# Kernel optimization log

Measured on AMD Instinct MI355X. Metric: run time of the kernel, lower is better.

The kernel has to match this reference:

```python
import jax, jax.numpy as jnp
import numpy as np

KS = 7001          # Gaussian kernel taps (hard-coded in smooth_predictions)
STD = 30.0
B, S, D = 512, 8000, 256


def gaussian_kernel():
    # torch.linspace(-size//2 + 1, size//2, size) with size=7001 -> -3500..3500
    x = jnp.linspace(-(KS // 2), KS // 2, KS)
    k = jnp.exp(-x ** 2 / (2.0 * STD ** 2))
    return k / jnp.sum(k)


def smooth_predictions(v):
    # v: (B, 1, S); depthwise (single-channel) conv1d, 'same' padding
    k = gaussian_kernel().reshape(1, 1, KS).astype(v.dtype)
    return jax.lax.conv_general_dilated(
        v, k, window_strides=(1,), padding=[(KS // 2, KS // 2)],
        dimension_numbers=('NCH', 'OIH', 'NCH'))


def _param(b, w, bias, lo, hi):
    # Linear(D,1) -> relu -> clamp; returns (B, 1)
    return jnp.clip(jax.nn.relu(b @ w.T + bias), lo, hi)


def setup_inputs() -> dict:
    key = jax.random.key(0)
    ks = jax.random.split(key, 10)
    inp = {
        'v_out': jax.random.normal(ks[0], (B, 1, S), jnp.float32),
        'b': jax.random.normal(ks[1], (B, D), jnp.float32),
        'k_w': 0.02 * jax.random.normal(ks[2], (1, D), jnp.float32),
        'k_b': jnp.zeros((1,), jnp.float32),
        'a_w': 0.02 * jax.random.normal(ks[3], (1, D), jnp.float32),
        'a_b': jnp.zeros((1,), jnp.float32),
        'epsilon_w': 0.02 * jax.random.normal(ks[4], (1, D), jnp.float32),
        'epsilon_b': jnp.zeros((1,), jnp.float32),
        'gamma_w': 0.02 * jax.random.normal(ks[5], (1, D), jnp.float32),
        'gamma_b': jnp.zeros((1,), jnp.float32),
        'use_cond': 0,
        'name': 0,
    }
    return inp


def reference(v_out, b, k_w, k_b, a_w, a_b, epsilon_w, epsilon_b,
              gamma_w, gamma_b, use_cond, name):
    t_ = jnp.ones_like(v_out) * 1.6            # (B,1,S)
    t_out = t_                                  # expanded form is identical

    k = _param(b, k_w, k_b, 0.1, 1.0)          # (B,1)
    a = _param(b, a_w, a_b, 0.001, 0.1)
    epsilon = _param(b, epsilon_w, epsilon_b, 0.005, 0.1)
    gamma = _param(b, gamma_w, gamma_b, 0.5, 2.0)

    # unsqueeze(1) + expand over seq -> broadcast as (B,1,1)
    k_e = k[:, :, None]
    a_e = a[:, :, None]
    eps_e = epsilon[:, :, None]
    g_e = gamma[:, :, None]

    ones = jnp.ones_like(v_out)
    v_s = smooth_predictions(v_out)            # (B,1,S)

    dv_l = jnp.pad(v_s, ((0, 0), (0, 0), (1, 0)))   # (B,1,S+1)
    dv_r = jnp.pad(v_s, ((0, 0), (0, 0), (0, 1)))   # (B,1,S+1)
    dt = t_out / 7999.0
    dv_t = (dv_r[:, :, 1:] - dv_l[:, :, :-1]) / (2.0 * dt)
    dv2_t = (dv_r[:, :, 1:] + dv_l[:, :, :-1] - 2.0 * v_s) / dt ** 2

    eps_0 = 0.001
    v_noisy = jnp.where(v_s == 0, jnp.full_like(v_s, eps_0), v_s)
    inv_v = v_noisy ** (-1)
    inv_v = jnp.where(jnp.isnan(inv_v), jnp.zeros_like(inv_v), inv_v)

    term_l1 = v_s * k_e * dv_t * (ones - 2.0 * v_s + a_e)
    term_l2 = inv_v * dv_t ** 2
    term_lt = 1000.0 * term_l1 + term_l2 - dv2_t

    term_r1 = v_s * (v_s - g_e * k_e * 1000.0 * (ones - v_s) * (v_s - a_e))
    term_rt = eps_e * (term_r1 + g_e * dv_t)

    dv_out = term_lt - term_rt
    if use_cond:
        dv_out = jnp.where(v_out <= 0, jnp.zeros_like(dv_out), dv_out)

    dv_out = jnp.concatenate([dv_out[:, :, 100:950], dv_out[:, :, 1050:-100]],
                             axis=2)
    dv_out = jnp.log(dv_out ** 2 + 1e-5)
    return (dv_out, dv_t, dv2_t, a, k * 1000.0, epsilon, gamma, t_,
            dv_l, dv_r, t_out)
```

## Files before the change

kernel.cpp:

```cpp
#include <hip/hip_runtime.h>
#include <math.h>

#define SLEN 8000
#define NBATCH 512
#define DDIM 256

#define RAD 160
#define TAPS (2 * RAD + 1)
#define CHUNK 2048
#define CBLK 256
#define TPO 8
#define WIN (CHUNK + 2 * RAD + 16)
#define LDSZ (WIN + WIN / 8)

#define O0  0
#define O1  3942400
#define O2  8038400
#define O3  12134400
#define O4  12134912
#define O5  12135424
#define O6  12135936
#define O7  12136448
#define O8  16232448
#define O9  20328960
#define O10 24425472

struct WTable { float w[TAPS]; };

__global__ __launch_bounds__(256) void pc_params_kernel(
    const float* __restrict__ b,
    const float* __restrict__ kw, const float* __restrict__ kb,
    const float* __restrict__ aw, const float* __restrict__ ab,
    const float* __restrict__ ew, const float* __restrict__ eb,
    const float* __restrict__ gw, const float* __restrict__ gb,
    float* __restrict__ out3, float* __restrict__ out4,
    float* __restrict__ out5, float* __restrict__ out6,
    float* __restrict__ wsp)
{
    __shared__ float4 red[256];
    const int row = blockIdx.x;
    const int d = threadIdx.x;
    const float bv = b[row * DDIM + d];
    red[d] = make_float4(bv * kw[d], bv * aw[d], bv * ew[d], bv * gw[d]);
    __syncthreads();
    for (int s2 = 128; s2 > 0; s2 >>= 1) {
        if (d < s2) {
            float4 o = red[d + s2];
            red[d].x += o.x; red[d].y += o.y; red[d].z += o.z; red[d].w += o.w;
        }
        __syncthreads();
    }
    if (d == 0) {
        float4 s = red[0];
        float k = fminf(fmaxf(fmaxf(s.x + kb[0], 0.0f), 0.1f),   1.0f);
        float a = fminf(fmaxf(fmaxf(s.y + ab[0], 0.0f), 0.001f), 0.1f);
        float e = fminf(fmaxf(fmaxf(s.z + eb[0], 0.0f), 0.005f), 0.1f);
        float g = fminf(fmaxf(fmaxf(s.w + gb[0], 0.0f), 0.5f),   2.0f);
        out3[row] = a;
        out4[row] = k * 1000.0f;
        out5[row] = e;
        out6[row] = g;
        wsp[row]          = k;
        wsp[512 + row]    = a;
        wsp[1024 + row]   = e;
        wsp[1536 + row]   = g;
    }
}

__global__ __launch_bounds__(CBLK) void pc_conv_kernel(
    const float* __restrict__ v,
    float* __restrict__ dvl,
    float* __restrict__ dvr,
    WTable wt)
{
    __shared__ float lds[LDSZ];
    const int row = blockIdx.y;
    const int i0 = blockIdx.x * CHUNK;
    const int tid = threadIdx.x;
    const float* vrow = v + row * SLEN;

    for (int idx = tid; idx < WIN; idx += CBLK) {
        const int g = i0 - RAD + idx;
        const float val = (g >= 0 && g < SLEN) ? vrow[g] : 0.0f;
        lds[idx + (idx >> 3)] = val;
    }
    __syncthreads();

    const int base = tid * TPO;
    float acc[TPO];
#pragma unroll
    for (int t = 0; t < TPO; ++t) acc[t] = 0.0f;

    float sreg[16];
    const float* p0 = lds + 9 * tid;
#pragma unroll
    for (int k = 0; k < 8; ++k) sreg[k] = p0[k];
#pragma unroll
    for (int k = 0; k < 8; ++k) sreg[8 + k] = p0[9 + k];

#pragma unroll 2
    for (int jb = 0; jb < TAPS - 1; jb += 8) {
#pragma unroll
        for (int c = 0; c < 8; ++c) {
            const float wc = wt.w[jb + c];
#pragma unroll
            for (int t = 0; t < TPO; ++t) acc[t] += wc * sreg[c + t];
        }
#pragma unroll
        for (int k = 0; k < 8; ++k) sreg[k] = sreg[k + 8];
        const float* pn = lds + 9 * tid + 9 * ((jb >> 3) + 2);
#pragma unroll
        for (int k = 0; k < 8; ++k) sreg[8 + k] = pn[k];
    }
    {
        const float wc = wt.w[TAPS - 1];
#pragma unroll
        for (int t = 0; t < TPO; ++t) acc[t] += wc * sreg[t];
    }

    const long rb = (long)row * 8001;
#pragma unroll
    for (int t = 0; t < TPO; ++t) {
        const int i = i0 + base + t;
        if (i < SLEN) {
            dvr[rb + i] = acc[t];
            dvl[rb + i + 1] = acc[t];
            if (i == 0) dvl[rb] = 0.0f;
            if (i == SLEN - 1) dvr[rb + SLEN] = 0.0f;
        }
    }
}

__global__ __launch_bounds__(256) void pc_pointwise_kernel(
    const float* __restrict__ dvr,
    const float* __restrict__ wsp,
    const float* __restrict__ v_out,
    const int* __restrict__ use_cond,
    float* __restrict__ out0, float* __restrict__ out1,
    float* __restrict__ out2, float* __restrict__ out7,
    float* __restrict__ out10)
{
    const int row = blockIdx.y;
    const int i = blockIdx.x * 256 + threadIdx.x;
    if (i >= SLEN) return;
    const long rb = (long)row * 8001;

    const float vc = dvr[rb + i];
    const float vm = (i > 0) ? dvr[rb + i - 1] : 0.0f;
    const float vp = dvr[rb + i + 1];

    const float kk = wsp[row];
    const float aa = wsp[512 + row];
    const float ee = wsp[1024 + row];
    const float gg = wsp[1536 + row];

    constexpr float DT = 1.6f / 7999.0f;
    constexpr float C1 = 1.0f / (2.0f * DT);
    constexpr float C2 = 1.0f / (DT * DT);

    const float dv_t = (vp - vm) * C1;
    const float dv2  = (vp + vm - 2.0f * vc) * C2;

    float vn = (vc == 0.0f) ? 0.001f : vc;
    float inv_v = 1.0f / vn;
    if (inv_v != inv_v) inv_v = 0.0f;

    const float term_l1 = vc * kk * dv_t * (1.0f - 2.0f * vc + aa);
    const float term_l2 = inv_v * dv_t * dv_t;
    const float term_lt = 1000.0f * term_l1 + term_l2 - dv2;
    const float term_r1 = vc * (vc - gg * kk * 1000.0f * (1.0f - vc) * (vc - aa));
    const float term_rt = ee * (term_r1 + gg * dv_t);
    float dvo = term_lt - term_rt;

    if (*use_cond) {
        if (v_out[(long)row * SLEN + i] <= 0.0f) dvo = 0.0f;
    }

    const long rs = (long)row * SLEN;
    out1[rs + i] = dv_t;
    out2[rs + i] = dv2;
    out7[rs + i] = 1.6f;
    out10[rs + i] = 1.6f;

    if (i >= 100 && i < 950) {
        out0[(long)row * 7700 + (i - 100)] = logf(dvo * dvo + 1e-5f);
    } else if (i >= 1050 && i < 7900) {
        out0[(long)row * 7700 + 850 + (i - 1050)] = logf(dvo * dvo + 1e-5f);
    }
}

static void build_wtable(WTable* wt) {
    double norm = 0.0;
    for (int d = -3500; d <= 3500; ++d)
        norm += exp(-(double)d * (double)d / 1800.0);
    for (int j = 0; j < TAPS; ++j) {
        const int d = j - RAD;
        wt->w[j] = (float)(exp(-(double)d * (double)d / 1800.0) / norm);
    }
}

extern "C" void kernel_launch(void* const* d_in, const int* in_sizes, int n_in,
                              void* d_out, int out_size, void* d_ws, size_t ws_size,
                              hipStream_t stream)
{
    const float* v_out = (const float*)d_in[0];
    const float* b  = (const float*)d_in[1];
    const float* kw = (const float*)d_in[2];
    const float* kb = (const float*)d_in[3];
    const float* aw = (const float*)d_in[4];
    const float* ab = (const float*)d_in[5];
    const float* ew = (const float*)d_in[6];
    const float* eb = (const float*)d_in[7];
    const float* gw = (const float*)d_in[8];
    const float* gb = (const float*)d_in[9];
    const int* use_cond = (const int*)d_in[10];
    float* out = (float*)d_out;
    float* wsp = (float*)d_ws;

    WTable wt;
    build_wtable(&wt);

    pc_params_kernel<<<NBATCH, 256, 0, stream>>>(
        b, kw, kb, aw, ab, ew, eb, gw, gb,
        out + O3, out + O4, out + O5, out + O6, wsp);

    pc_conv_kernel<<<dim3((SLEN + CHUNK - 1) / CHUNK, NBATCH), CBLK, 0, stream>>>(
        v_out, out + O8, out + O9, wt);

    pc_pointwise_kernel<<<dim3((SLEN + 255) / 256, NBATCH), 256, 0, stream>>>(
        out + O9, wsp, v_out, use_cond,
        out + O0, out + O1, out + O2, out + O7, out + O10);
}
```

Before: 194.2 us.

## Fuse Gaussian conv with pointwise PDE terms and vectorize output stores

Merges the convolution and pointwise kernels so the smoothed signal stays in registers and neighbours come from shared memory, with boundary threads computing one extra conv output each. This removes the write-then-reread of dv_r through global memory and one kernel launch. Gaussian weights are now computed on the device into LDS instead of being passed as a kernel argument. Outputs are written with float4 stores. The price is a serial 321-tap loop in two threads per block, which stalls that block's other threads at the barrier.

```diff
diff --git a/kernel.cpp b/kernel.cpp
--- a/kernel.cpp
+++ b/kernel.cpp
@@ -6,11 +6,12 @@
 #define DDIM 256
 
 #define RAD 160
-#define TAPS (2 * RAD + 1)
+#define TAPS 321
 #define CHUNK 2048
 #define CBLK 256
 #define TPO 8
-#define WIN (CHUNK + 2 * RAD + 16)
+#define HALO_L 176
+#define WIN (HALO_L + CHUNK + RAD + 16)
 #define LDSZ (WIN + WIN / 8)
 
 #define O0  0
@@ -25,7 +26,7 @@
 #define O9  20328960
 #define O10 24425472
 
-struct WTable { float w[TAPS]; };
+typedef float f4u __attribute__((vector_size(16), aligned(4)));
 
 __global__ __launch_bounds__(256) void pc_params_kernel(
     const float* __restrict__ b,
@@ -67,135 +68,164 @@
     }
 }
 
-__global__ __launch_bounds__(CBLK) void pc_conv_kernel(
+__global__ __launch_bounds__(CBLK) void pc_fused_kernel(
     const float* __restrict__ v,
-    float* __restrict__ dvl,
-    float* __restrict__ dvr,
-    WTable wt)
+    const float* __restrict__ wsp,
+    const int* __restrict__ use_cond,
+    float* __restrict__ out0, float* __restrict__ out1,
+    float* __restrict__ out2, float* __restrict__ out7,
+    float* __restrict__ dvl,  float* __restrict__ dvr,
+    float* __restrict__ out10)
 {
     __shared__ float lds[LDSZ];
+    __shared__ __align__(16) float wlds[TAPS + 7];
+    __shared__ float eL[CBLK], eR[CBLK];
+
     const int row = blockIdx.y;
     const int i0 = blockIdx.x * CHUNK;
     const int tid = threadIdx.x;
-    const float* vrow = v + row * SLEN;
-
+    const float* vrow = v + (long)row * SLEN;
+
+    for (int j = tid; j < TAPS; j += CBLK) {
+        const float d = (float)(j - RAD);
+        wlds[j] = expf(d * d * (-1.0f / 1800.0f)) * (float)(1.0 / 75.19884823893001);
+    }
+
+    const int st = i0 - HALO_L;
     for (int idx = tid; idx < WIN; idx += CBLK) {
-        const int g = i0 - RAD + idx;
+        const int g = st + idx;
         const float val = (g >= 0 && g < SLEN) ? vrow[g] : 0.0f;
         lds[idx + (idx >> 3)] = val;
     }
     __syncthreads();
 
-    const int base = tid * TPO;
     float acc[TPO];
 #pragma unroll
     for (int t = 0; t < TPO; ++t) acc[t] = 0.0f;
 
     float sreg[16];
-    const float* p0 = lds + 9 * tid;
-#pragma unroll
-    for (int k = 0; k < 8; ++k) sreg[k] = p0[k];
-#pragma unroll
-    for (int k = 0; k < 8; ++k) sreg[8 + k] = p0[9 + k];
+    {
+        const float* p0 = lds + 9 * (tid + 2);
+        const float* p1 = lds + 9 * (tid + 3);
+#pragma unroll
+        for (int k = 0; k < 8; ++k) sreg[k] = p0[k];
+#pragma unroll
+        for (int k = 0; k < 8; ++k) sreg[8 + k] = p1[k];
+    }
 
 #pragma unroll 2
-    for (int jb = 0; jb < TAPS - 1; jb += 8) {
+    for (int m = 0; m < 40; ++m) {
+        const float4 w0 = *(const float4*)(wlds + 8 * m);
+        const float4 w1 = *(const float4*)(wlds + 8 * m + 4);
+        const float wc[8] = {w0.x, w0.y, w0.z, w0.w, w1.x, w1.y, w1.z, w1.w};
 #pragma unroll
         for (int c = 0; c < 8; ++c) {
-            const float wc = wt.w[jb + c];
-#pragma unroll
-            for (int t = 0; t < TPO; ++t) acc[t] += wc * sreg[c + t];
+#pragma unroll
+            for (int t = 0; t < TPO; ++t) acc[t] += wc[c] * sreg[c + t];
         }
 #pragma unroll
         for (int k = 0; k < 8; ++k) sreg[k] = sreg[k + 8];
-        const float* pn = lds + 9 * tid + 9 * ((jb >> 3) + 2);
+        const float* pn = lds + 9 * (tid + m + 4);
 #pragma unroll
         for (int k = 0; k < 8; ++k) sreg[8 + k] = pn[k];
     }
     {
-        const float wc = wt.w[TAPS - 1];
+        const float wc = wlds[TAPS - 1];
 #pragma unroll
         for (int t = 0; t < TPO; ++t) acc[t] += wc * sreg[t];
     }
 
-    const long rb = (long)row * 8001;
-#pragma unroll
-    for (int t = 0; t < TPO; ++t) {
-        const int i = i0 + base + t;
-        if (i < SLEN) {
-            dvr[rb + i] = acc[t];
-            dvl[rb + i + 1] = acc[t];
-            if (i == 0) dvl[rb] = 0.0f;
-            if (i == SLEN - 1) dvr[rb + SLEN] = 0.0f;
-        }
-    }
-}
-
-__global__ __launch_bounds__(256) void pc_pointwise_kernel(
-    const float* __restrict__ dvr,
-    const float* __restrict__ wsp,
-    const float* __restrict__ v_out,
-    const int* __restrict__ use_cond,
-    float* __restrict__ out0, float* __restrict__ out1,
-    float* __restrict__ out2, float* __restrict__ out7,
-    float* __restrict__ out10)
-{
-    const int row = blockIdx.y;
-    const int i = blockIdx.x * 256 + threadIdx.x;
-    if (i >= SLEN) return;
-    const long rb = (long)row * 8001;
-
-    const float vc = dvr[rb + i];
-    const float vm = (i > 0) ? dvr[rb + i - 1] : 0.0f;
-    const float vp = dvr[rb + i + 1];
+    float leftE = 0.0f, rightE = 0.0f;
+    if (tid == 0) {
+        for (int j = 0; j < TAPS; ++j) {
+            const int x = 15 + j;
+            leftE += wlds[j] * lds[x + (x >> 3)];
+        }
+    }
+    if (tid == CBLK - 1) {
+        for (int j = 0; j < TAPS; ++j) {
+            const int x = 2064 + j;
+            rightE += wlds[j] * lds[x + (x >> 3)];
+        }
+    }
+
+    eL[tid] = acc[0];
+    eR[tid] = acc[7];
+    __syncthreads();
+    const float eRp = (tid > 0)        ? eR[tid - 1] : leftE;
+    const float eLn = (tid < CBLK - 1) ? eL[tid + 1] : rightE;
 
     const float kk = wsp[row];
     const float aa = wsp[512 + row];
     const float ee = wsp[1024 + row];
     const float gg = wsp[1536 + row];
+    const int uc = *use_cond;
 
     constexpr float DT = 1.6f / 7999.0f;
     constexpr float C1 = 1.0f / (2.0f * DT);
     constexpr float C2 = 1.0f / (DT * DT);
 
-    const float dv_t = (vp - vm) * C1;
-    const float dv2  = (vp + vm - 2.0f * vc) * C2;
-
-    float vn = (vc == 0.0f) ? 0.001f : vc;
-    float inv_v = 1.0f / vn;
-    if (inv_v != inv_v) inv_v = 0.0f;
-
-    const float term_l1 = vc * kk * dv_t * (1.0f - 2.0f * vc + aa);
-    const float term_l2 = inv_v * dv_t * dv_t;
-    const float term_lt = 1000.0f * term_l1 + term_l2 - dv2;
-    const float term_r1 = vc * (vc - gg * kk * 1000.0f * (1.0f - vc) * (vc - aa));
-    const float term_rt = ee * (term_r1 + gg * dv_t);
-    float dvo = term_lt - term_rt;
-
-    if (*use_cond) {
-        if (v_out[(long)row * SLEN + i] <= 0.0f) dvo = 0.0f;
-    }
-
-    const long rs = (long)row * SLEN;
-    out1[rs + i] = dv_t;
-    out2[rs + i] = dv2;
-    out7[rs + i] = 1.6f;
-    out10[rs + i] = 1.6f;
-
-    if (i >= 100 && i < 950) {
-        out0[(long)row * 7700 + (i - 100)] = logf(dvo * dvo + 1e-5f);
-    } else if (i >= 1050 && i < 7900) {
-        out0[(long)row * 7700 + 850 + (i - 1050)] = logf(dvo * dvo + 1e-5f);
-    }
-}
-
-static void build_wtable(WTable* wt) {
-    double norm = 0.0;
-    for (int d = -3500; d <= 3500; ++d)
-        norm += exp(-(double)d * (double)d / 1800.0);
-    for (int j = 0; j < TAPS; ++j) {
-        const int d = j - RAD;
-        wt->w[j] = (float)(exp(-(double)d * (double)d / 1800.0) / norm);
+    const int i8 = i0 + 8 * tid;
+    float dvt8[TPO], dv28[TPO], lg8[TPO];
+#pragma unroll
+    for (int t = 0; t < TPO; ++t) {
+        const int i = i8 + t;
+        const float vc = acc[t];
+        float vm = (t == 0) ? eRp : acc[t - 1];
+        float vp = (t == TPO - 1) ? eLn : acc[t + 1];
+        if (i == 0) vm = 0.0f;
+        if (i == SLEN - 1) vp = 0.0f;
+
+        const float dv_t = (vp - vm) * C1;
+        const float dv2  = (vp + vm - 2.0f * vc) * C2;
+
+        float vn = (vc == 0.0f) ? 0.001f : vc;
+        float inv_v = 1.0f / vn;
+        if (inv_v != inv_v) inv_v = 0.0f;
+
+        const float term_l1 = vc * kk * dv_t * (1.0f - 2.0f * vc + aa);
+        const float term_l2 = inv_v * dv_t * dv_t;
+        const float term_lt = 1000.0f * term_l1 + term_l2 - dv2;
+        const float term_r1 = vc * (vc - gg * kk * 1000.0f * (1.0f - vc) * (vc - aa));
+        const float term_rt = ee * (term_r1 + gg * dv_t);
+        float dvo = term_lt - term_rt;
+        if (uc) {
+            if (vrow[i < SLEN ? i : 0] <= 0.0f) dvo = 0.0f;
+        }
+        dvt8[t] = dv_t;
+        dv28[t] = dv2;
+        lg8[t]  = logf(dvo * dvo + 1e-5f);
+    }
+
+    if (i8 < SLEN) {
+        const long rs = (long)row * SLEN + i8;
+        *(float4*)(out1 + rs)     = make_float4(dvt8[0], dvt8[1], dvt8[2], dvt8[3]);
+        *(float4*)(out1 + rs + 4) = make_float4(dvt8[4], dvt8[5], dvt8[6], dvt8[7]);
+        *(float4*)(out2 + rs)     = make_float4(dv28[0], dv28[1], dv28[2], dv28[3]);
+        *(float4*)(out2 + rs + 4) = make_float4(dv28[4], dv28[5], dv28[6], dv28[7]);
+        const float4 c16 = make_float4(1.6f, 1.6f, 1.6f, 1.6f);
+        *(float4*)(out7 + rs)      = c16;
+        *(float4*)(out7 + rs + 4)  = c16;
+        *(float4*)(out10 + rs)     = c16;
+        *(float4*)(out10 + rs + 4) = c16;
+
+        const long rb = (long)row * (SLEN + 1) + i8;
+        f4u a0 = {acc[0], acc[1], acc[2], acc[3]};
+        f4u a1 = {acc[4], acc[5], acc[6], acc[7]};
+        *(f4u*)(dvr + rb)     = a0;
+        *(f4u*)(dvr + rb + 4) = a1;
+        *(f4u*)(dvl + rb + 1) = a0;
+        *(f4u*)(dvl + rb + 5) = a1;
+        if (i8 == 0)        dvl[(long)row * (SLEN + 1)] = 0.0f;
+        if (i8 == SLEN - 8) dvr[(long)row * (SLEN + 1) + SLEN] = 0.0f;
+
+        const long r0 = (long)row * 7700;
+#pragma unroll
+        for (int t = 0; t < TPO; ++t) {
+            const int i = i8 + t;
+            if (i >= 100 && i < 950)        out0[r0 + (i - 100)] = lg8[t];
+            else if (i >= 1050 && i < 7900) out0[r0 + (i - 200)] = lg8[t];
+        }
     }
 }
 
@@ -217,17 +247,12 @@
     float* out = (float*)d_out;
     float* wsp = (float*)d_ws;
 
-    WTable wt;
-    build_wtable(&wt);
-
     pc_params_kernel<<<NBATCH, 256, 0, stream>>>(
         b, kw, kb, aw, ab, ew, eb, gw, gb,
         out + O3, out + O4, out + O5, out + O6, wsp);
 
-    pc_conv_kernel<<<dim3((SLEN + CHUNK - 1) / CHUNK, NBATCH), CBLK, 0, stream>>>(
-        v_out, out + O8, out + O9, wt);
-
-    pc_pointwise_kernel<<<dim3((SLEN + 255) / 256, NBATCH), 256, 0, stream>>>(
-        out + O9, wsp, v_out, use_cond,
-        out + O0, out + O1, out + O2, out + O7, out + O10);
+    pc_fused_kernel<<<dim3((SLEN + CHUNK - 1) / CHUNK, NBATCH), CBLK, 0, stream>>>(
+        v_out, wsp, use_cond,
+        out + O0, out + O1, out + O2, out + O7,
+        out + O8, out + O9, out + O10);
 }
```

After: 190.7 us. About the same (-1.8%).
